# Kernel tuning notes

Measured on AMD Instinct MI355X. Metric: run time of the kernel, lower is better.

Reference implementation:

```python
import jax, jax.numpy as jnp
import numpy as np

N = 100000   # nodes
H = 96       # hidden_dim
A = 32       # attn_dim
De = 16      # edge_embeddings_dim
E = 500000   # edges per edge type
NEG_SLOPE = 0.01  # torch F.leaky_relu default


def setup_inputs() -> dict:
    key = jax.random.key(0)
    ks = jax.random.split(key, 24)
    nrm = lambda k, shape, s=1.0: jax.random.normal(k, shape, dtype=jnp.float32) * s
    idx = lambda k: jax.random.randint(k, (E,), 0, N, dtype=jnp.int32)
    Din = 2 * H + De
    return {
        'h': nrm(ks[0], (N, H)),
        'src0': idx(ks[1]), 'dst0': idx(ks[2]),
        'src1': idx(ks[3]), 'dst1': idx(ks[4]),
        'src2': idx(ks[5]), 'dst2': idx(ks[6]),
        'Wm0': nrm(ks[7], (Din, H), Din ** -0.5), 'bm0': jnp.zeros((H,), jnp.float32), 'ef0': nrm(ks[8], (De,)),
        'Wm1': nrm(ks[9], (Din, H), Din ** -0.5), 'bm1': jnp.zeros((H,), jnp.float32), 'ef1': nrm(ks[10], (De,)),
        'Wm2': nrm(ks[11], (Din, H), Din ** -0.5), 'bm2': jnp.zeros((H,), jnp.float32), 'ef2': nrm(ks[12], (De,)),
        'Wn0': nrm(ks[13], (H, A), H ** -0.5), 'Wa0': nrm(ks[14], (2 * A, 1), (2 * A) ** -0.5),
        'Wn1': nrm(ks[15], (H, A), H ** -0.5), 'Wa1': nrm(ks[16], (2 * A, 1), (2 * A) ** -0.5),
        'Wu': nrm(ks[17], (4 * H, H), (4 * H) ** -0.5), 'bu': jnp.zeros((H,), jnp.float32),
    }


def _leaky(x):
    return jnp.where(x > 0, x, NEG_SLOPE * x)


def _edge_msg(h, src, dst, Wm, bm, ef):
    # cat(src_h, dst_h, edge_feature) -> Linear  (dropout p=0, eval mode)
    x = jnp.concatenate([h[src], h[dst], jnp.broadcast_to(ef, (src.shape[0], ef.shape[0]))], axis=-1)
    return x @ Wm + bm  # [E, H]


def _mean_agg(m, dst):
    # fn.mean('m','msg'): per-destination mean over incoming edges
    s = jax.ops.segment_sum(m, dst, num_segments=N)
    c = jax.ops.segment_sum(jnp.ones((m.shape[0],), m.dtype), dst, num_segments=N)
    return s / jnp.maximum(c, 1.0)[:, None]


def _attn_agg(scores, m, dst):
    # per-destination softmax over mailbox (variable-size), then weighted sum
    smax = jax.ops.segment_max(scores, dst, num_segments=N)
    ex = jnp.exp(scores - smax[dst])
    den = jax.ops.segment_sum(ex, dst, num_segments=N)
    num = jax.ops.segment_sum(ex[:, None] * m, dst, num_segments=N)
    return num / jnp.maximum(den, 1e-9)[:, None]


def reference(h, src0, dst0, src1, dst1, src2, dst2,
              Wm0, bm0, ef0, Wm1, bm1, ef1, Wm2, bm2, ef2,
              Wn0, Wa0, Wn1, Wa1, Wu, bu):
    # edge type 0: intra_diff (attention), type 1: inter_diff (attention), type 2: intra_lt (mean)
    m0 = _edge_msg(h, src0, dst0, Wm0, bm0, ef0)
    m1 = _edge_msg(h, src1, dst1, Wm1, bm1, ef1)
    m2 = _edge_msg(h, src2, dst2, Wm2, bm2, ef2)

    z0 = h @ Wn0  # [N, A]
    s0 = _leaky(jnp.concatenate([z0[src0], z0[dst0]], axis=-1) @ Wa0)[:, 0]  # [E]
    z1 = h @ Wn1
    s1 = _leaky(jnp.concatenate([z1[src1], z1[dst1]], axis=-1) @ Wa1)[:, 0]

    msg0 = _attn_agg(s0, m0, dst0)   # [N, H]
    msg1 = _attn_agg(s1, m1, dst1)
    msg2 = _mean_agg(m2, dst2)

    # cross_reducer='stack' then concat over edge-type dim -> [N, 3H]
    mcat = jnp.concatenate([msg0, msg1, msg2], axis=-1)
    # cell node update: Linear(cat(h, m)) + ReLU
    return jax.nn.relu(jnp.concatenate([h, mcat], axis=-1) @ Wu + bu)
```

## Files before the change

### kernel.cpp

```cpp
#include <hip/hip_runtime.h>
#include <hip/hip_bf16.h>
#include <cstdint>

#define NN 100000
#define HH 96
#define AD 32
#define DE 16
#define EE 500000
#define NEG 0.01f

#define GSH 10
#define GSZ 1024
#define KB 98
#define CH 4096
#define BPT 123

typedef __bf16 bf16x8 __attribute__((ext_vector_type(8)));
typedef float  f32x4  __attribute__((ext_vector_type(4)));
typedef unsigned long long ull;

__device__ __forceinline__ unsigned short f2b(float x) {
    union { float f; unsigned int u; } v; v.f = x;
    unsigned int r = v.u + 0x7fffu + ((v.u >> 16) & 1u);
    return (unsigned short)(r >> 16);
}
__device__ __forceinline__ float b2f(unsigned short h) {
    union { unsigned int u; float f; } v; v.u = ((unsigned int)h) << 16;
    return v.f;
}

__global__ void prep_kernel(const float* Wm0, const float* bm0, const float* ef0,
                            const float* Wm1, const float* bm1, const float* ef1,
                            const float* Wm2, const float* bm2, const float* ef2,
                            const float* Wn0, const float* Wa0,
                            const float* Wn1, const float* Wa1,
                            const float* Wu,
                            float* cvec, float* wvec,
                            unsigned short* BfN, unsigned short* BfU) {
    const float* Wm[3] = {Wm0, Wm1, Wm2};
    const float* bm[3] = {bm0, bm1, bm2};
    const float* ef[3] = {ef0, ef1, ef2};
    const int total = 288 + 384 + 55296 + 36864;
    for (int i = blockIdx.x * blockDim.x + threadIdx.x; i < total;
         i += gridDim.x * blockDim.x) {
        if (i < 288) {
            int t = i / 96, j = i % 96;
            float s = bm[t][j];
            for (int k = 0; k < DE; ++k) s += ef[t][k] * Wm[t][(2 * HH + k) * HH + j];
            cvec[i] = s;
        } else if (i < 288 + 384) {
            int ii = i - 288;
            int kind = ii / 96, k = ii % 96;
            const float* Wn = (kind < 2) ? Wn0 : Wn1;
            const float* Wa = (kind < 2) ? Wa0 : Wa1;
            int off = (kind & 1) ? AD : 0;
            float s = 0.f;
            for (int a = 0; a < AD; ++a) s += Wn[k * AD + a] * Wa[off + a];
            wvec[ii] = s;
        } else if (i < 288 + 384 + 55296) {
            int ii = i - 672;
            int sec = ii / 9216; int rem = ii % 9216;
            int ksc = rem / 512; int lj = rem % 512;
            int ks = ksc / 6, c = ksc % 6;
            int lane = lj / 8, jj = lj % 8;
            int quad = lane / 16, m = lane % 16;
            int k = ks * 32 + quad * 8 + jj;
            int n = c * 16 + m;
            int mt = (sec < 3) ? sec : sec - 3;
            int rowoff = (sec < 3) ? 0 : HH;
            BfN[ii] = f2b(Wm[mt][(rowoff + k) * HH + n]);
        } else {
            int ii = i - (672 + 55296);
            int ksc = ii / 512; int lj = ii % 512;
            int ks = ksc / 6, c = ksc % 6;
            int lane = lj / 8, jj = lj % 8;
            int quad = lane / 16, m = lane % 16;
            int k = ks * 32 + quad * 8 + jj;
            int n = c * 16 + m;
            BfU[ii] = f2b(Wu[k * HH + n]);
        }
    }
}

__global__ void cast_uv_kernel(const float* __restrict__ h, const float* __restrict__ wvec,
                               unsigned short* __restrict__ hb, float* __restrict__ uv) {
    int lane = threadIdx.x & 31;
    int node = (blockIdx.x * blockDim.x + threadIdx.x) >> 5;
    if (node >= NN) return;
    float h0 = h[node * HH + lane];
    float h1 = h[node * HH + 32 + lane];
    float h2 = h[node * HH + 64 + lane];
    hb[node * HH + lane] = f2b(h0);
    hb[node * HH + 32 + lane] = f2b(h1);
    hb[node * HH + 64 + lane] = f2b(h2);
    float acc[4];
#pragma unroll
    for (int q = 0; q < 4; ++q)
        acc[q] = h0 * wvec[q * 96 + lane] + h1 * wvec[q * 96 + 32 + lane] +
                 h2 * wvec[q * 96 + 64 + lane];
#pragma unroll
    for (int d = 16; d >= 1; d >>= 1)
#pragma unroll
        for (int q = 0; q < 4; ++q) acc[q] += __shfl_down(acc[q], d, 32);
    if (lane == 0) {
#pragma unroll
        for (int q = 0; q < 4; ++q) uv[q * NN + node] = acc[q];
    }
}

__global__ void zero_kernel(float4* __restrict__ p, int n4) {
    for (int i = blockIdx.x * blockDim.x + threadIdx.x; i < n4;
         i += gridDim.x * blockDim.x)
        p[i] = make_float4(0.f, 0.f, 0.f, 0.f);
}

__global__ void bucket_hist(const int* __restrict__ s0, const int* __restrict__ d0,
                            const int* __restrict__ s1, const int* __restrict__ d1,
                            const int* __restrict__ s2, const int* __restrict__ d2,
                            const float* __restrict__ uv,
                            int* __restrict__ bCnt, float* __restrict__ wtmp) {
    __shared__ int hist[3 * KB];
    int t = threadIdx.x;
    for (int j = t; j < 3 * KB; j += 256) hist[j] = 0;
    __syncthreads();
    const int total = 3 * EE;
    for (int i = blockIdx.x * blockDim.x + t; i < total; i += gridDim.x * blockDim.x) {
        int ty = i / EE, e = i - ty * EE;
        const int* dp = (ty == 0) ? d0 : (ty == 1) ? d1 : d2;
        int d = dp[e];
        atomicAdd(&hist[ty * KB + (d >> GSH)], 1);
        if (ty < 2) {
            const int* sp = (ty == 0) ? s0 : s1;
            int s = sp[e];
            float c = uv[2 * ty * NN + s] + uv[(2 * ty + 1) * NN + d];
            c = c > 0.f ? c : NEG * c;
            wtmp[(size_t)ty * EE + e] = __expf(c);
        }
    }
    __syncthreads();
    for (int j = t; j < 3 * KB; j += 256)
        if (hist[j]) atomicAdd(&bCnt[j], hist[j]);
}

__global__ void bucket_scan(const int* __restrict__ bCnt, int* __restrict__ bBase,
                            int* __restrict__ gCursor, int* __restrict__ rs,
                            ull* __restrict__ wrec) {
    __shared__ int hist[3 * KB];
    int t = threadIdx.x;
    if (t < 3 * KB) hist[t] = bCnt[t];
    if (t < 8) wrec[(size_t)3 * EE + t] = 0ull;
    __syncthreads();
    if (t < 3) {
        int run = 0;
        for (int b = 0; b < KB; ++b) {
            bBase[t * (KB + 1) + b] = run;
            gCursor[t * KB + b] = run;
            run += hist[t * KB + b];
        }
        bBase[t * (KB + 1) + KB] = run;
        rs[(size_t)t * (NN + 1) + NN] = run;
    }
}

__global__ __launch_bounds__(256) void bucket_scatter(
    const int* __restrict__ s0, const int* __restrict__ d0,
    const int* __restrict__ s1, const int* __restrict__ d1,
    const int* __restrict__ s2, const int* __restrict__ d2,
    const float* __restrict__ wtmp,
    int* __restrict__ gCursor, ull* __restrict__ binned) {
    __shared__ ull recs[CH];
    __shared__ unsigned short rnk[CH];
    __shared__ unsigned char bkt[CH];
    __shared__ int cnt[KB];
    __shared__ int gpos[KB];
    int t = threadIdx.x;
    int type = blockIdx.x / BPT;
    int chunk = (blockIdx.x % BPT) * CH;
    const int* src = (type == 0) ? s0 : (type == 1) ? s1 : s2;
    const int* dst = (type == 0) ? d0 : (type == 1) ? d1 : d2;
    if (t < KB) cnt[t] = 0;
    __syncthreads();
#pragma unroll
    for (int k = 0; k < CH / 256; ++k) {
        int idx = k * 256 + t;
        int e = chunk + idx;
        if (e < EE) {
            int s = src[e], d = dst[e];
            int b = d >> GSH;
            float w = (type < 2) ? wtmp[(size_t)type * EE + e] : 1.0f;
            recs[idx] = ((ull)__float_as_uint(w) << 32) |
                        ((unsigned int)s << GSH) | (unsigned int)(d & (GSZ - 1));
            bkt[idx] = (unsigned char)b;
            rnk[idx] = (unsigned short)atomicAdd(&cnt[b], 1);
        } else {
            bkt[idx] = 0xFF;
        }
    }
    __syncthreads();
    if (t < KB) {
        int c = cnt[t];
        gpos[t] = (c > 0) ? atomicAdd(&gCursor[type * KB + t], c) : 0;
    }
    __syncthreads();
    ull* bout = binned + (size_t)type * EE;
#pragma unroll
    for (int k = 0; k < CH / 256; ++k) {
        int idx = k * 256 + t;
        unsigned char b = bkt[idx];
        if (b != 0xFF) bout[gpos[b] + rnk[idx]] = recs[idx];
    }
}

__global__ __launch_bounds__(256) void bucket_sort(
    const ull* __restrict__ binned, const int* __restrict__ bBase,
    int* __restrict__ rs, ull* __restrict__ wrec) {
    __shared__ int cnt[GSZ];
    __shared__ int tsum[256];
    int t = threadIdx.x;
    int type = blockIdx.x / KB;
    int b = blockIdx.x % KB;
    int nodeBase = b * GSZ;
    int eb = bBase[type * (KB + 1) + b];
    int en = bBase[type * (KB + 1) + b + 1];
    int n = en - eb;
    const ull* bin = binned + (size_t)type * EE + eb;
    const unsigned int* binlo = (const unsigned int*)bin;
#pragma unroll
    for (int k = 0; k < GSZ / 256; ++k) cnt[k * 256 + t] = 0;
    __syncthreads();
    for (int i = t; i < n; i += 256) atomicAdd(&cnt[binlo[2 * i] & (GSZ - 1)], 1);
    __syncthreads();
    int v[4], s = 0;
#pragma unroll
    for (int k = 0; k < 4; ++k) { v[k] = cnt[t * 4 + k]; s += v[k]; }
    tsum[t] = s;
    __syncthreads();
    for (int off = 1; off < 256; off <<= 1) {
        int add = (t >= off) ? tsum[t - off] : 0;
        __syncthreads();
        tsum[t] += add;
        __syncthreads();
    }
    int run = tsum[t] - s;
    int offk[4];
#pragma unroll
    for (int k = 0; k < 4; ++k) { offk[k] = run; run += v[k]; }
    int* rsrow = rs + (size_t)type * (NN + 1) + nodeBase;
#pragma unroll
    for (int k = 0; k < 4; ++k) {
        int node = t * 4 + k;
        if (nodeBase + node < NN) rsrow[node] = eb + offk[k];
    }
    __syncthreads();
#pragma unroll
    for (int k = 0; k < 4; ++k) cnt[t * 4 + k] = offk[k];
    __syncthreads();
    ull* wo = wrec + (size_t)type * EE + eb;
    for (int i = t; i < n; i += 256) {
        ull r = bin[i];
        unsigned int lo = (unsigned int)r;
        int dl = lo & (GSZ - 1);
        int p = atomicAdd(&cnt[dl], 1);
        unsigned int off = (lo >> GSH) * 192u;
        wo[p] = (r & 0xFFFFFFFF00000000ull) | (ull)off;
    }
}

__global__ void aggregate_kernel(const int* __restrict__ rsAll,
                                 const ull* __restrict__ wrec,
                                 const unsigned short* __restrict__ hb,
                                 unsigned short* __restrict__ hagg,
                                 float* __restrict__ den) {
    const size_t NH = (size_t)NN * HH;
    int lane = threadIdx.x & 31;
    int node = (blockIdx.x * blockDim.x + threadIdx.x) >> 5;
    if (node >= NN) return;
    int t = blockIdx.y;
    const int* rs = rsAll + (size_t)t * (NN + 1);
    const ull* wr = wrec + (size_t)t * EE;
    int beg = rs[node], end = rs[node + 1];
    float a0 = 0.f, a1 = 0.f, a2 = 0.f, dn = 0.f;
    const char* b0 = (const char*)hb + 4 * lane;
    const char* b1 = (const char*)hb + 128 + 2 * lane;
#define EDGE(rec, cond)                                                        \
    {                                                                          \
        float w = (cond) ? __uint_as_float((unsigned int)((rec) >> 32)) : 0.f; \
        unsigned int off = (unsigned int)(rec);                                \
        unsigned int dv = *(const unsigned int*)(b0 + off);                    \
        unsigned int sv = *(const unsigned short*)(b1 + off);                  \
        a0 += w * __uint_as_float(dv << 16);                                   \
        a1 += w * __uint_as_float(dv & 0xFFFF0000u);                           \
        a2 += w * __uint_as_float(sv << 16);                                   \
        dn += w;                                                               \
    }
    for (int j = beg; j < end; j += 4) {
        ull r0 = wr[j], r1 = wr[j + 1], r2 = wr[j + 2], r3 = wr[j + 3];
        EDGE(r0, true);
        EDGE(r1, j + 1 < end);
        EDGE(r2, j + 2 < end);
        EDGE(r3, j + 3 < end);
    }
#undef EDGE
    float inv = (dn > 0.f) ? 1.f / dn : 0.f;
    float q0 = a0 * inv, q1 = a1 * inv, q2 = a2 * inv;
    char* mr = (char*)(hagg + (size_t)t * NH + (size_t)node * HH);
    *(unsigned int*)(mr + 4 * lane) =
        (unsigned int)f2b(q0) | ((unsigned int)f2b(q1) << 16);
    *(unsigned short*)(mr + 128 + 2 * lane) = f2b(q2);
    if (lane == 0) den[(size_t)t * NN + node] = dn;
}

__global__ __launch_bounds__(256) void msg_gemm_kernel(const unsigned short* __restrict__ hagg,
                                                       const unsigned short* __restrict__ hb,
                                                       const unsigned short* __restrict__ BfN,
                                                       const float* __restrict__ den,
                                                       const float* __restrict__ cvec,
                                                       unsigned short* __restrict__ msgb) {
    const size_t NH = (size_t)NN * HH;
    int wave = threadIdx.x >> 6;
    int lane = threadIdx.x & 63;
    int quad = lane >> 4, m = lane & 15;
    int blk = blockIdx.x * 4 + wave;
    if (blk >= NN / 16) return;
    int t = blockIdx.y;
    int r0 = blk * 16;
    const unsigned short* ha = hagg + (size_t)t * NH;
    f32x4 acc[6] = {};
#pragma unroll
    for (int ks = 0; ks < 6; ++ks) {
        const unsigned short* ap =
            (ks < 3) ? ha + (size_t)(r0 + m) * HH + ks * 32 + quad * 8
                     : hb + (size_t)(r0 + m) * HH + (ks - 3) * 32 + quad * 8;
        int sec = (ks < 3) ? t : t + 3;
        int kk = (ks < 3) ? ks : ks - 3;
        bf16x8 af = *(const bf16x8*)ap;
#pragma unroll
        for (int c = 0; c < 6; ++c) {
            bf16x8 bfv = *(const bf16x8*)(BfN + (((sec * 3 + kk) * 6 + c) << 9) + lane * 8);
            acc[c] = __builtin_amdgcn_mfma_f32_16x16x32_bf16(af, bfv, acc[c], 0, 0, 0);
        }
    }
    float dn[4];
#pragma unroll
    for (int r = 0; r < 4; ++r) dn[r] = den[(size_t)t * NN + r0 + quad * 4 + r];
#pragma unroll
    for (int c = 0; c < 6; ++c) {
        float cv = cvec[t * 96 + c * 16 + m];
#pragma unroll
        for (int r = 0; r < 4; ++r) {
            int row = r0 + quad * 4 + r;
            float val = (dn[r] > 0.f) ? (acc[c][r] + cv) : 0.f;
            msgb[(size_t)row * 288 + t * 96 + c * 16 + m] = f2b(val);
        }
    }
}

__global__ __launch_bounds__(256) void update_gemm_kernel(const unsigned short* __restrict__ hb,
                                                          const unsigned short* __restrict__ msgb,
                                                          const unsigned short* __restrict__ BfU,
                                                          const float* __restrict__ bu,
                                                          float* __restrict__ out) {
    int wave = threadIdx.x >> 6;
    int lane = threadIdx.x & 63;
    int quad = lane >> 4, m = lane & 15;
    int blk = blockIdx.x * 4 + wave;
    if (blk >= NN / 16) return;
    int r0 = blk * 16;
    f32x4 acc[6] = {};
#pragma unroll
    for (int ks = 0; ks < 12; ++ks) {
        const unsigned short* ap =
            (ks < 3) ? hb + (size_t)(r0 + m) * HH + ks * 32 + quad * 8
                     : msgb + (size_t)(r0 + m) * 288 + (ks - 3) * 32 + quad * 8;
        bf16x8 af = *(const bf16x8*)ap;
#pragma unroll
        for (int c = 0; c < 6; ++c) {
            bf16x8 bfv = *(const bf16x8*)(BfU + ((ks * 6 + c) << 9) + lane * 8);
            acc[c] = __builtin_amdgcn_mfma_f32_16x16x32_bf16(af, bfv, acc[c], 0, 0, 0);
        }
    }
#pragma unroll
    for (int c = 0; c < 6; ++c) {
        float b = bu[c * 16 + m];
#pragma unroll
        for (int r = 0; r < 4; ++r) {
            int row = r0 + quad * 4 + r;
            float v2 = acc[c][r] + b;
            out[(size_t)row * HH + c * 16 + m] = v2 > 0.f ? v2 : 0.f;
        }
    }
}

extern "C" void kernel_launch(void* const* d_in, const int* in_sizes, int n_in,
                              void* d_out, int out_size, void* d_ws, size_t ws_size,
                              hipStream_t stream) {
    (void)in_sizes; (void)n_in; (void)out_size;
    const float* h   = (const float*)d_in[0];
    const int* srcs[3] = {(const int*)d_in[1], (const int*)d_in[3], (const int*)d_in[5]};
    const int* dsts[3] = {(const int*)d_in[2], (const int*)d_in[4], (const int*)d_in[6]};
    const float* Wm0 = (const float*)d_in[7];
    const float* bm0 = (const float*)d_in[8];
    const float* ef0 = (const float*)d_in[9];
    const float* Wm1 = (const float*)d_in[10];
    const float* bm1 = (const float*)d_in[11];
    const float* ef1 = (const float*)d_in[12];
    const float* Wm2 = (const float*)d_in[13];
    const float* bm2 = (const float*)d_in[14];
    const float* ef2 = (const float*)d_in[15];
    const float* Wn0 = (const float*)d_in[16];
    const float* Wa0 = (const float*)d_in[17];
    const float* Wn1 = (const float*)d_in[18];
    const float* Wa1 = (const float*)d_in[19];
    const float* Wu  = (const float*)d_in[20];
    const float* bu  = (const float*)d_in[21];
    float* out = (float*)d_out;

    const size_t NEED = 166591232;
    if (ws_size < NEED) return;
    char* w = (char*)d_ws;
    unsigned short* msgb    = (unsigned short*)(w + 0);
    unsigned short* hb      = (unsigned short*)(w + 57600000);
    unsigned short* hagg    = (unsigned short*)(w + 76800000);
    float*          den     = (float*)(w + 134400000);
    float*          uv      = (float*)(w + 135600000);
    float*          cvec    = (float*)(w + 137200000);
    float*          wvec    = (float*)(w + 137201280);
    unsigned short* BfN     = (unsigned short*)(w + 137202816);
    unsigned short* BfU     = (unsigned short*)(w + 137313408);
    int*            bBase   = (int*)(w + 137387136);
    int*            gCursor = (int*)(w + 137388416);
    int*            bCnt    = (int*)(w + 137389696);
    int*            rs      = (int*)(w + 137390976);
    ull*            wrec    = (ull*)(w + 138591104);
    ull*            binned  = (ull*)(w + 150591232);
    float*          wtmp    = (float*)(w + 162591232);

    prep_kernel<<<128, 256, 0, stream>>>(Wm0, bm0, ef0, Wm1, bm1, ef1, Wm2, bm2, ef2,
                                         Wn0, Wa0, Wn1, Wa1, Wu, cvec, wvec, BfN, BfU);
    cast_uv_kernel<<<12500, 256, 0, stream>>>(h, wvec, hb, uv);

    zero_kernel<<<1, 256, 0, stream>>>((float4*)bCnt, 80);
    bucket_hist<<<512, 256, 0, stream>>>(srcs[0], dsts[0], srcs[1], dsts[1],
                                         srcs[2], dsts[2], uv, bCnt, wtmp);
    bucket_scan<<<1, 384, 0, stream>>>(bCnt, bBase, gCursor, rs, wrec);
    bucket_scatter<<<3 * BPT, 256, 0, stream>>>(srcs[0], dsts[0], srcs[1], dsts[1],
                                                srcs[2], dsts[2], wtmp, gCursor, binned);
    bucket_sort<<<3 * KB, 256, 0, stream>>>(binned, bBase, rs, wrec);

    aggregate_kernel<<<dim3(12500, 3), 256, 0, stream>>>(rs, wrec, hb, hagg, den);
    msg_gemm_kernel<<<dim3(1563, 3), 256, 0, stream>>>(hagg, hb, BfN, den, cvec, msgb);
    update_gemm_kernel<<<1563, 256, 0, stream>>>(hb, msgb, BfU, bu, out);
}
```

Baseline: 331.1 us.

## Defer attention weight compute to bucket sort and degree-sort aggregation nodes

```diff
diff --git a/kernel.cpp b/kernel.cpp
--- a/kernel.cpp
+++ b/kernel.cpp
@@ -114,11 +114,8 @@
         p[i] = make_float4(0.f, 0.f, 0.f, 0.f);
 }
 
-__global__ void bucket_hist(const int* __restrict__ s0, const int* __restrict__ d0,
-                            const int* __restrict__ s1, const int* __restrict__ d1,
-                            const int* __restrict__ s2, const int* __restrict__ d2,
-                            const float* __restrict__ uv,
-                            int* __restrict__ bCnt, float* __restrict__ wtmp) {
+__global__ void bucket_hist(const int* __restrict__ d0, const int* __restrict__ d1,
+                            const int* __restrict__ d2, int* __restrict__ bCnt) {
     __shared__ int hist[3 * KB];
     int t = threadIdx.x;
     for (int j = t; j < 3 * KB; j += 256) hist[j] = 0;
@@ -126,16 +123,8 @@
     const int total = 3 * EE;
     for (int i = blockIdx.x * blockDim.x + t; i < total; i += gridDim.x * blockDim.x) {
         int ty = i / EE, e = i - ty * EE;
-        const int* dp = (ty == 0) ? d0 : (ty == 1) ? d1 : d2;
-        int d = dp[e];
-        atomicAdd(&hist[ty * KB + (d >> GSH)], 1);
-        if (ty < 2) {
-            const int* sp = (ty == 0) ? s0 : s1;
-            int s = sp[e];
-            float c = uv[2 * ty * NN + s] + uv[(2 * ty + 1) * NN + d];
-            c = c > 0.f ? c : NEG * c;
-            wtmp[(size_t)ty * EE + e] = __expf(c);
-        }
+        const int* d = (ty == 0) ? d0 : (ty == 1) ? d1 : d2;
+        atomicAdd(&hist[ty * KB + (d[e] >> GSH)], 1);
     }
     __syncthreads();
     for (int j = t; j < 3 * KB; j += 256)
@@ -144,11 +133,12 @@
 
 __global__ void bucket_scan(const int* __restrict__ bCnt, int* __restrict__ bBase,
                             int* __restrict__ gCursor, int* __restrict__ rs,
-                            ull* __restrict__ wrec) {
+                            ull* __restrict__ wrec, int* __restrict__ clsCnt) {
     __shared__ int hist[3 * KB];
     int t = threadIdx.x;
     if (t < 3 * KB) hist[t] = bCnt[t];
     if (t < 8) wrec[(size_t)3 * EE + t] = 0ull;
+    if (t < 48) clsCnt[t] = 0;
     __syncthreads();
     if (t < 3) {
         int run = 0;
@@ -166,9 +156,8 @@
     const int* __restrict__ s0, const int* __restrict__ d0,
     const int* __restrict__ s1, const int* __restrict__ d1,
     const int* __restrict__ s2, const int* __restrict__ d2,
-    const float* __restrict__ wtmp,
-    int* __restrict__ gCursor, ull* __restrict__ binned) {
-    __shared__ ull recs[CH];
+    int* __restrict__ gCursor, unsigned int* __restrict__ binned) {
+    __shared__ unsigned int recs[CH];
     __shared__ unsigned short rnk[CH];
     __shared__ unsigned char bkt[CH];
     __shared__ int cnt[KB];
@@ -187,9 +176,7 @@
         if (e < EE) {
             int s = src[e], d = dst[e];
             int b = d >> GSH;
-            float w = (type < 2) ? wtmp[(size_t)type * EE + e] : 1.0f;
-            recs[idx] = ((ull)__float_as_uint(w) << 32) |
-                        ((unsigned int)s << GSH) | (unsigned int)(d & (GSZ - 1));
+            recs[idx] = ((unsigned int)s << GSH) | (unsigned int)(d & (GSZ - 1));
             bkt[idx] = (unsigned char)b;
             rnk[idx] = (unsigned short)atomicAdd(&cnt[b], 1);
         } else {
@@ -202,7 +189,7 @@
         gpos[t] = (c > 0) ? atomicAdd(&gCursor[type * KB + t], c) : 0;
     }
     __syncthreads();
-    ull* bout = binned + (size_t)type * EE;
+    unsigned int* bout = binned + (size_t)type * EE;
 #pragma unroll
     for (int k = 0; k < CH / 256; ++k) {
         int idx = k * 256 + t;
@@ -212,10 +199,13 @@
 }
 
 __global__ __launch_bounds__(256) void bucket_sort(
-    const ull* __restrict__ binned, const int* __restrict__ bBase,
-    int* __restrict__ rs, ull* __restrict__ wrec) {
+    const unsigned int* __restrict__ binned, const int* __restrict__ bBase,
+    const float* __restrict__ uv,
+    int* __restrict__ rs, ull* __restrict__ wrec, int* __restrict__ clsCnt) {
     __shared__ int cnt[GSZ];
     __shared__ int tsum[256];
+    __shared__ float vbuf[GSZ];
+    __shared__ int lcls[16];
     int t = threadIdx.x;
     int type = blockIdx.x / KB;
     int b = blockIdx.x % KB;
@@ -223,12 +213,20 @@
     int eb = bBase[type * (KB + 1) + b];
     int en = bBase[type * (KB + 1) + b + 1];
     int n = en - eb;
-    const ull* bin = binned + (size_t)type * EE + eb;
-    const unsigned int* binlo = (const unsigned int*)bin;
+    const unsigned int* bin = binned + (size_t)type * EE + eb;
 #pragma unroll
     for (int k = 0; k < GSZ / 256; ++k) cnt[k * 256 + t] = 0;
-    __syncthreads();
-    for (int i = t; i < n; i += 256) atomicAdd(&cnt[binlo[2 * i] & (GSZ - 1)], 1);
+    if (t < 16) lcls[t] = 0;
+    if (type < 2) {
+        const float* vsrc = uv + (2 * type + 1) * NN;
+#pragma unroll
+        for (int k = 0; k < GSZ / 256; ++k) {
+            int nd = nodeBase + k * 256 + t;
+            vbuf[k * 256 + t] = (nd < NN) ? vsrc[nd] : 0.f;
+        }
+    }
+    __syncthreads();
+    for (int i = t; i < n; i += 256) atomicAdd(&cnt[bin[i] & (GSZ - 1)], 1);
     __syncthreads();
     int v[4], s = 0;
 #pragma unroll
@@ -249,33 +247,84 @@
 #pragma unroll
     for (int k = 0; k < 4; ++k) {
         int node = t * 4 + k;
-        if (nodeBase + node < NN) rsrow[node] = eb + offk[k];
+        if (nodeBase + node < NN) {
+            rsrow[node] = eb + offk[k];
+            int cls = (v[k] + 3) >> 2;
+            if (cls > 15) cls = 15;
+            atomicAdd(&lcls[cls], 1);
+        }
     }
     __syncthreads();
 #pragma unroll
     for (int k = 0; k < 4; ++k) cnt[t * 4 + k] = offk[k];
     __syncthreads();
+    if (t < 16 && lcls[t]) atomicAdd(&clsCnt[type * 16 + t], lcls[t]);
     ull* wo = wrec + (size_t)type * EE + eb;
+    const float* usrc = uv + 2 * type * NN;
     for (int i = t; i < n; i += 256) {
-        ull r = bin[i];
-        unsigned int lo = (unsigned int)r;
-        int dl = lo & (GSZ - 1);
+        unsigned int r = bin[i];
+        int dl = r & (GSZ - 1);
         int p = atomicAdd(&cnt[dl], 1);
-        unsigned int off = (lo >> GSH) * 192u;
-        wo[p] = (r & 0xFFFFFFFF00000000ull) | (ull)off;
-    }
+        unsigned int sidx = r >> GSH;
+        float w = 1.f;
+        if (type < 2) {
+            float c = usrc[sidx] + vbuf[dl];
+            c = fmaxf(c, NEG * c);
+            w = __expf(c);
+        }
+        wo[p] = ((ull)__float_as_uint(w) << 32) | (ull)(sidx * 192u);
+    }
+}
+
+__global__ void perm_scan(const int* __restrict__ clsCnt, int* __restrict__ cursor) {
+    int t = threadIdx.x;
+    if (t < 3) {
+        int run = t * NN;
+        for (int c = 0; c < 16; ++c) {
+            cursor[t * 16 + c] = run;
+            run += clsCnt[t * 16 + c];
+        }
+    }
+}
+
+__global__ __launch_bounds__(256) void perm_scatter(const int* __restrict__ rs,
+                                                    int* __restrict__ cursor,
+                                                    int* __restrict__ perm) {
+    __shared__ int lh[48];
+    __shared__ int lbase[48];
+    int t = threadIdx.x;
+    int i = blockIdx.x * 256 + t;
+    if (t < 48) lh[t] = 0;
+    __syncthreads();
+    int cidx = -1, rnkv = 0, node = 0;
+    if (i < 3 * NN) {
+        int type = i / NN;
+        node = i - type * NN;
+        const int* r = rs + (size_t)type * (NN + 1) + node;
+        int deg = r[1] - r[0];
+        int cls = (deg + 3) >> 2;
+        if (cls > 15) cls = 15;
+        cidx = type * 16 + cls;
+        rnkv = atomicAdd(&lh[cidx], 1);
+    }
+    __syncthreads();
+    if (t < 48) lbase[t] = lh[t] ? atomicAdd(&cursor[t], lh[t]) : 0;
+    __syncthreads();
+    if (cidx >= 0) perm[lbase[cidx] + rnkv] = node;
 }
 
 __global__ void aggregate_kernel(const int* __restrict__ rsAll,
+                                 const int* __restrict__ perm,
                                  const ull* __restrict__ wrec,
                                  const unsigned short* __restrict__ hb,
                                  unsigned short* __restrict__ hagg,
                                  float* __restrict__ den) {
     const size_t NH = (size_t)NN * HH;
     int lane = threadIdx.x & 31;
-    int node = (blockIdx.x * blockDim.x + threadIdx.x) >> 5;
-    if (node >= NN) return;
+    int g = (blockIdx.x * blockDim.x + threadIdx.x) >> 5;
+    if (g >= NN) return;
     int t = blockIdx.y;
+    int node = perm[t * NN + g];
     const int* rs = rsAll + (size_t)t * (NN + 1);
     const ull* wr = wrec + (size_t)t * EE;
     int beg = rs[node], end = rs[node + 1];
@@ -415,7 +464,7 @@
     const float* bu  = (const float*)d_in[21];
     float* out = (float*)d_out;
 
-    const size_t NEED = 166591232;
+    const size_t NEED = 157791616;
     if (ws_size < NEED) return;
     char* w = (char*)d_ws;
     unsigned short* msgb    = (unsigned short*)(w + 0);
@@ -432,22 +481,25 @@
     int*            bCnt    = (int*)(w + 137389696);
     int*            rs      = (int*)(w + 137390976);
     ull*            wrec    = (ull*)(w + 138591104);
-    ull*            binned  = (ull*)(w + 150591232);
-    float*          wtmp    = (float*)(w + 162591232);
+    unsigned int*   binned  = (unsigned int*)(w + 150591232);
+    int*            clsCnt  = (int*)(w + 156591232);
+    int*            cursor  = (int*)(w + 156591424);
+    int*            perm    = (int*)(w + 156591616);
 
     prep_kernel<<<128, 256, 0, stream>>>(Wm0, bm0, ef0, Wm1, bm1, ef1, Wm2, bm2, ef2,
                                          Wn0, Wa0, Wn1, Wa1, Wu, cvec, wvec, BfN, BfU);
     cast_uv_kernel<<<12500, 256, 0, stream>>>(h, wvec, hb, uv);
 
     zero_kernel<<<1, 256, 0, stream>>>((float4*)bCnt, 80);
-    bucket_hist<<<512, 256, 0, stream>>>(srcs[0], dsts[0], srcs[1], dsts[1],
-                                         srcs[2], dsts[2], uv, bCnt, wtmp);
-    bucket_scan<<<1, 384, 0, stream>>>(bCnt, bBase, gCursor, rs, wrec);
+    bucket_hist<<<512, 256, 0, stream>>>(dsts[0], dsts[1], dsts[2], bCnt);
+    bucket_scan<<<1, 384, 0, stream>>>(bCnt, bBase, gCursor, rs, wrec, clsCnt);
     bucket_scatter<<<3 * BPT, 256, 0, stream>>>(srcs[0], dsts[0], srcs[1], dsts[1],
-                                                srcs[2], dsts[2], wtmp, gCursor, binned);
-    bucket_sort<<<3 * KB, 256, 0, stream>>>(binned, bBase, rs, wrec);
-
-    aggregate_kernel<<<dim3(12500, 3), 256, 0, stream>>>(rs, wrec, hb, hagg, den);
+                                                srcs[2], dsts[2], gCursor, binned);
+    bucket_sort<<<3 * KB, 256, 0, stream>>>(binned, bBase, uv, rs, wrec, clsCnt);
+    perm_scan<<<1, 64, 0, stream>>>(clsCnt, cursor);
+    perm_scatter<<<1172, 256, 0, stream>>>(rs, cursor, perm);
+
+    aggregate_kernel<<<dim3(12500, 3), 256, 0, stream>>>(rs, perm, wrec, hb, hagg, den);
     msg_gemm_kernel<<<dim3(1563, 3), 256, 0, stream>>>(hagg, hb, BfN, den, cvec, msgb);
     update_gemm_kernel<<<1563, 256, 0, stream>>>(hb, msgb, BfU, bu, out);
 }
```

New measurement: 342.8 us. 3.5% more time.

## Replace two-level bucket sort with padded CSR built by global atomic scatter

Applied to the files above, without the earlier changes.

```diff
diff --git a/kernel.cpp b/kernel.cpp
--- a/kernel.cpp
+++ b/kernel.cpp
@@ -12,12 +12,12 @@
 #define GSH 10
 #define GSZ 1024
 #define KB 98
-#define CH 4096
-#define BPT 123
+#define PCAP 800000
 
 typedef __bf16 bf16x8 __attribute__((ext_vector_type(8)));
 typedef float  f32x4  __attribute__((ext_vector_type(4)));
 typedef unsigned long long ull;
+typedef unsigned long long ull2 __attribute__((ext_vector_type(2)));
 
 __device__ __forceinline__ unsigned short f2b(float x) {
     union { float f; unsigned int u; } v; v.f = x;
@@ -114,125 +114,32 @@
         p[i] = make_float4(0.f, 0.f, 0.f, 0.f);
 }
 
-__global__ void bucket_hist(const int* __restrict__ s0, const int* __restrict__ d0,
-                            const int* __restrict__ s1, const int* __restrict__ d1,
-                            const int* __restrict__ s2, const int* __restrict__ d2,
-                            const float* __restrict__ uv,
-                            int* __restrict__ bCnt, float* __restrict__ wtmp) {
-    __shared__ int hist[3 * KB];
-    int t = threadIdx.x;
-    for (int j = t; j < 3 * KB; j += 256) hist[j] = 0;
-    __syncthreads();
-    const int total = 3 * EE;
-    for (int i = blockIdx.x * blockDim.x + t; i < total; i += gridDim.x * blockDim.x) {
-        int ty = i / EE, e = i - ty * EE;
-        const int* dp = (ty == 0) ? d0 : (ty == 1) ? d1 : d2;
-        int d = dp[e];
-        atomicAdd(&hist[ty * KB + (d >> GSH)], 1);
-        if (ty < 2) {
-            const int* sp = (ty == 0) ? s0 : s1;
-            int s = sp[e];
-            float c = uv[2 * ty * NN + s] + uv[(2 * ty + 1) * NN + d];
-            c = c > 0.f ? c : NEG * c;
-            wtmp[(size_t)ty * EE + e] = __expf(c);
-        }
-    }
-    __syncthreads();
-    for (int j = t; j < 3 * KB; j += 256)
-        if (hist[j]) atomicAdd(&bCnt[j], hist[j]);
-}
-
-__global__ void bucket_scan(const int* __restrict__ bCnt, int* __restrict__ bBase,
-                            int* __restrict__ gCursor, int* __restrict__ rs,
-                            ull* __restrict__ wrec) {
-    __shared__ int hist[3 * KB];
-    int t = threadIdx.x;
-    if (t < 3 * KB) hist[t] = bCnt[t];
-    if (t < 8) wrec[(size_t)3 * EE + t] = 0ull;
-    __syncthreads();
-    if (t < 3) {
-        int run = 0;
-        for (int b = 0; b < KB; ++b) {
-            bBase[t * (KB + 1) + b] = run;
-            gCursor[t * KB + b] = run;
-            run += hist[t * KB + b];
-        }
-        bBase[t * (KB + 1) + KB] = run;
-        rs[(size_t)t * (NN + 1) + NN] = run;
-    }
-}
-
-__global__ __launch_bounds__(256) void bucket_scatter(
-    const int* __restrict__ s0, const int* __restrict__ d0,
-    const int* __restrict__ s1, const int* __restrict__ d1,
-    const int* __restrict__ s2, const int* __restrict__ d2,
-    const float* __restrict__ wtmp,
-    int* __restrict__ gCursor, ull* __restrict__ binned) {
-    __shared__ ull recs[CH];
-    __shared__ unsigned short rnk[CH];
-    __shared__ unsigned char bkt[CH];
-    __shared__ int cnt[KB];
-    __shared__ int gpos[KB];
-    int t = threadIdx.x;
-    int type = blockIdx.x / BPT;
-    int chunk = (blockIdx.x % BPT) * CH;
-    const int* src = (type == 0) ? s0 : (type == 1) ? s1 : s2;
-    const int* dst = (type == 0) ? d0 : (type == 1) ? d1 : d2;
-    if (t < KB) cnt[t] = 0;
-    __syncthreads();
-#pragma unroll
-    for (int k = 0; k < CH / 256; ++k) {
-        int idx = k * 256 + t;
-        int e = chunk + idx;
-        if (e < EE) {
-            int s = src[e], d = dst[e];
-            int b = d >> GSH;
-            float w = (type < 2) ? wtmp[(size_t)type * EE + e] : 1.0f;
-            recs[idx] = ((ull)__float_as_uint(w) << 32) |
-                        ((unsigned int)s << GSH) | (unsigned int)(d & (GSZ - 1));
-            bkt[idx] = (unsigned char)b;
-            rnk[idx] = (unsigned short)atomicAdd(&cnt[b], 1);
-        } else {
-            bkt[idx] = 0xFF;
-        }
-    }
-    __syncthreads();
-    if (t < KB) {
-        int c = cnt[t];
-        gpos[t] = (c > 0) ? atomicAdd(&gCursor[type * KB + t], c) : 0;
-    }
-    __syncthreads();
-    ull* bout = binned + (size_t)type * EE;
-#pragma unroll
-    for (int k = 0; k < CH / 256; ++k) {
-        int idx = k * 256 + t;
-        unsigned char b = bkt[idx];
-        if (b != 0xFF) bout[gpos[b] + rnk[idx]] = recs[idx];
-    }
-}
-
-__global__ __launch_bounds__(256) void bucket_sort(
-    const ull* __restrict__ binned, const int* __restrict__ bBase,
-    int* __restrict__ rs, ull* __restrict__ wrec) {
-    __shared__ int cnt[GSZ];
+__global__ void deg_hist(const int* __restrict__ d0, const int* __restrict__ d1,
+                         const int* __restrict__ d2, int* __restrict__ deg) {
+    int i = blockIdx.x * blockDim.x + threadIdx.x;
+    if (i >= 3 * EE) return;
+    int ty = i / EE, e = i - ty * EE;
+    const int* d = (ty == 0) ? d0 : (ty == 1) ? d1 : d2;
+    atomicAdd(&deg[ty * NN + d[e]], 1);
+}
+
+__global__ __launch_bounds__(256) void pad_scan1(const int* __restrict__ deg,
+                                                 int* __restrict__ loc,
+                                                 int* __restrict__ bSum) {
     __shared__ int tsum[256];
     int t = threadIdx.x;
-    int type = blockIdx.x / KB;
-    int b = blockIdx.x % KB;
+    int blk = blockIdx.x;
+    int type = blk / KB, b = blk % KB;
     int nodeBase = b * GSZ;
-    int eb = bBase[type * (KB + 1) + b];
-    int en = bBase[type * (KB + 1) + b + 1];
-    int n = en - eb;
-    const ull* bin = binned + (size_t)type * EE + eb;
-    const unsigned int* binlo = (const unsigned int*)bin;
-#pragma unroll
-    for (int k = 0; k < GSZ / 256; ++k) cnt[k * 256 + t] = 0;
-    __syncthreads();
-    for (int i = t; i < n; i += 256) atomicAdd(&cnt[binlo[2 * i] & (GSZ - 1)], 1);
-    __syncthreads();
+    const int* dg = deg + (size_t)type * NN;
     int v[4], s = 0;
 #pragma unroll
-    for (int k = 0; k < 4; ++k) { v[k] = cnt[t * 4 + k]; s += v[k]; }
+    for (int k = 0; k < 4; ++k) {
+        int node = nodeBase + t * 4 + k;
+        int dd = (node < NN) ? dg[node] : 0;
+        v[k] = (dd + 3) & ~3;
+        s += v[k];
+    }
     tsum[t] = s;
     __syncthreads();
     for (int off = 1; off < 256; off <<= 1) {
@@ -242,28 +149,68 @@
         __syncthreads();
     }
     int run = tsum[t] - s;
-    int offk[4];
-#pragma unroll
-    for (int k = 0; k < 4; ++k) { offk[k] = run; run += v[k]; }
-    int* rsrow = rs + (size_t)type * (NN + 1) + nodeBase;
+    int* lrow = loc + (size_t)type * NN;
 #pragma unroll
     for (int k = 0; k < 4; ++k) {
-        int node = t * 4 + k;
-        if (nodeBase + node < NN) rsrow[node] = eb + offk[k];
-    }
-    __syncthreads();
-#pragma unroll
-    for (int k = 0; k < 4; ++k) cnt[t * 4 + k] = offk[k];
-    __syncthreads();
-    ull* wo = wrec + (size_t)type * EE + eb;
-    for (int i = t; i < n; i += 256) {
-        ull r = bin[i];
-        unsigned int lo = (unsigned int)r;
-        int dl = lo & (GSZ - 1);
-        int p = atomicAdd(&cnt[dl], 1);
-        unsigned int off = (lo >> GSH) * 192u;
-        wo[p] = (r & 0xFFFFFFFF00000000ull) | (ull)off;
-    }
+        int node = nodeBase + t * 4 + k;
+        if (node < NN) lrow[node] = run;
+        run += v[k];
+    }
+    if (t == 255) bSum[blk] = tsum[255];
+}
+
+__global__ void pad_scan2(const int* __restrict__ bSum, int* __restrict__ bBase,
+                          int* __restrict__ rs) {
+    int t = threadIdx.x;
+    if (t < 3) {
+        int run = 0;
+        for (int b = 0; b < KB; ++b) {
+            bBase[t * (KB + 1) + b] = run;
+            run += bSum[t * KB + b];
+        }
+        bBase[t * (KB + 1) + KB] = run;
+        rs[(size_t)t * (NN + 1) + NN] = run;
+    }
+}
+
+__global__ __launch_bounds__(256) void pad_finalize(const int* __restrict__ deg,
+                                                    const int* __restrict__ bBase,
+                                                    int* __restrict__ loc_cursor,
+                                                    int* __restrict__ rs,
+                                                    ull* __restrict__ wrec) {
+    int i = blockIdx.x * 256 + threadIdx.x;
+    if (i >= 3 * NN) return;
+    int type = i / NN, node = i - type * NN;
+    int b = node >> GSH;
+    int base = bBase[type * (KB + 1) + b] + loc_cursor[i];
+    rs[(size_t)type * (NN + 1) + node] = base;
+    loc_cursor[i] = base;
+    int dd = deg[i];
+    int psz = (dd + 3) & ~3;
+    ull* wp = wrec + (size_t)type * PCAP + base;
+    for (int k = dd; k < psz; ++k) wp[k] = 0ull;
+}
+
+__global__ void scatter_w(const int* __restrict__ s0, const int* __restrict__ d0,
+                          const int* __restrict__ s1, const int* __restrict__ d1,
+                          const int* __restrict__ s2, const int* __restrict__ d2,
+                          const float* __restrict__ uv,
+                          int* __restrict__ cursor, ull* __restrict__ wrec) {
+    int i = blockIdx.x * blockDim.x + threadIdx.x;
+    if (i >= 3 * EE) return;
+    int ty = i / EE, e = i - ty * EE;
+    const int* sp = (ty == 0) ? s0 : (ty == 1) ? s1 : s2;
+    const int* dp = (ty == 0) ? d0 : (ty == 1) ? d1 : d2;
+    int s = sp[e], d = dp[e];
+    float w = 1.f;
+    if (ty < 2) {
+        float c = uv[2 * ty * NN + s] + uv[(2 * ty + 1) * NN + d];
+        c = fmaxf(c, NEG * c);
+        w = __expf(c);
+    }
+    int p = atomicAdd(&cursor[ty * NN + d], 1);
+    wrec[(size_t)ty * PCAP + p] =
+        ((ull)__float_as_uint(w) << 32) | (ull)((unsigned int)s * 192u);
 }
 
 __global__ void aggregate_kernel(const int* __restrict__ rsAll,
@@ -277,14 +224,14 @@
     if (node >= NN) return;
     int t = blockIdx.y;
     const int* rs = rsAll + (size_t)t * (NN + 1);
-    const ull* wr = wrec + (size_t)t * EE;
+    const ull* wr = wrec + (size_t)t * PCAP;
     int beg = rs[node], end = rs[node + 1];
     float a0 = 0.f, a1 = 0.f, a2 = 0.f, dn = 0.f;
     const char* b0 = (const char*)hb + 4 * lane;
     const char* b1 = (const char*)hb + 128 + 2 * lane;
-#define EDGE(rec, cond)                                                        \
+#define EDGE(rec)                                                              \
     {                                                                          \
-        float w = (cond) ? __uint_as_float((unsigned int)((rec) >> 32)) : 0.f; \
+        float w = __uint_as_float((unsigned int)((rec) >> 32));                \
         unsigned int off = (unsigned int)(rec);                                \
         unsigned int dv = *(const unsigned int*)(b0 + off);                    \
         unsigned int sv = *(const unsigned short*)(b1 + off);                  \
@@ -294,11 +241,12 @@
         dn += w;                                                               \
     }
     for (int j = beg; j < end; j += 4) {
-        ull r0 = wr[j], r1 = wr[j + 1], r2 = wr[j + 2], r3 = wr[j + 3];
-        EDGE(r0, true);
-        EDGE(r1, j + 1 < end);
-        EDGE(r2, j + 2 < end);
-        EDGE(r3, j + 3 < end);
+        ull2 p0 = *(const ull2*)(wr + j);
+        ull2 p1 = *(const ull2*)(wr + j + 2);
+        EDGE(p0[0]);
+        EDGE(p0[1]);
+        EDGE(p1[0]);
+        EDGE(p1[1]);
     }
 #undef EDGE
     float inv = (dn > 0.f) ? 1.f / dn : 0.f;
@@ -415,7 +363,7 @@
     const float* bu  = (const float*)d_in[21];
     float* out = (float*)d_out;
 
-    const size_t NEED = 166591232;
+    const size_t NEED = 160189824;
     if (ws_size < NEED) return;
     char* w = (char*)d_ws;
     unsigned short* msgb    = (unsigned short*)(w + 0);
@@ -427,25 +375,24 @@
     float*          wvec    = (float*)(w + 137201280);
     unsigned short* BfN     = (unsigned short*)(w + 137202816);
     unsigned short* BfU     = (unsigned short*)(w + 137313408);
-    int*            bBase   = (int*)(w + 137387136);
-    int*            gCursor = (int*)(w + 137388416);
-    int*            bCnt    = (int*)(w + 137389696);
-    int*            rs      = (int*)(w + 137390976);
-    ull*            wrec    = (ull*)(w + 138591104);
-    ull*            binned  = (ull*)(w + 150591232);
-    float*          wtmp    = (float*)(w + 162591232);
+    int*            rs      = (int*)(w + 137387136);
+    int*            deg     = (int*)(w + 138587264);
+    int*            cursor  = (int*)(w + 139787264);
+    int*            bSum    = (int*)(w + 140987264);
+    int*            bBase   = (int*)(w + 140988544);
+    ull*            wrec    = (ull*)(w + 140989824);
 
     prep_kernel<<<128, 256, 0, stream>>>(Wm0, bm0, ef0, Wm1, bm1, ef1, Wm2, bm2, ef2,
                                          Wn0, Wa0, Wn1, Wa1, Wu, cvec, wvec, BfN, BfU);
     cast_uv_kernel<<<12500, 256, 0, stream>>>(h, wvec, hb, uv);
 
-    zero_kernel<<<1, 256, 0, stream>>>((float4*)bCnt, 80);
-    bucket_hist<<<512, 256, 0, stream>>>(srcs[0], dsts[0], srcs[1], dsts[1],
-                                         srcs[2], dsts[2], uv, bCnt, wtmp);
-    bucket_scan<<<1, 384, 0, stream>>>(bCnt, bBase, gCursor, rs, wrec);
-    bucket_scatter<<<3 * BPT, 256, 0, stream>>>(srcs[0], dsts[0], srcs[1], dsts[1],
-                                                srcs[2], dsts[2], wtmp, gCursor, binned);
-    bucket_sort<<<3 * KB, 256, 0, stream>>>(binned, bBase, rs, wrec);
+    zero_kernel<<<293, 256, 0, stream>>>((float4*)deg, 75000);
+    deg_hist<<<5860, 256, 0, stream>>>(dsts[0], dsts[1], dsts[2], deg);
+    pad_scan1<<<3 * KB, 256, 0, stream>>>(deg, cursor, bSum);
+    pad_scan2<<<1, 64, 0, stream>>>(bSum, bBase, rs);
+    pad_finalize<<<1172, 256, 0, stream>>>(deg, bBase, cursor, rs, wrec);
+    scatter_w<<<5860, 256, 0, stream>>>(srcs[0], dsts[0], srcs[1], dsts[1],
+                                        srcs[2], dsts[2], uv, cursor, wrec);
 
     aggregate_kernel<<<dim3(12500, 3), 256, 0, stream>>>(rs, wrec, hb, hagg, den);
     msg_gemm_kernel<<<dim3(1563, 3), 256, 0, stream>>>(hagg, hb, BfN, den, cvec, msgb);
```

Measured after the change: 412.8 us. 1.25x slower.
